# Kernel tuning notes

Measured on AMD Instinct MI355X. Metric: run time of the kernel, lower is better.

Reference implementation:

```python
import jax, jax.numpy as jnp
import numpy as np

B, C, N = 8, 512, 2048
C8 = C // 8


def setup_inputs() -> dict:
    key = jax.random.key(0)
    kx, kq, kk, kv, kg = jax.random.split(key, 5)
    return {
        "x": jax.random.normal(kx, (B, C, N), dtype=jnp.float32),
        "Wq": jax.random.normal(kq, (C8, C), dtype=jnp.float32) * (1.0 / np.sqrt(C)),
        "Wk": jax.random.normal(kk, (C8, C), dtype=jnp.float32) * (1.0 / np.sqrt(C)),
        "Wv": jax.random.normal(kv, (C, C), dtype=jnp.float32) * (1.0 / np.sqrt(C)),
        # torch init is gamma=0.0; use a small random value so the attention
        # branch contributes to the output.
        "gamma": jax.random.uniform(kg, (1,), dtype=jnp.float32),
    }


def reference(x, Wq, Wk, Wv, gamma):
    # 1x1 convs == per-position linear maps over channels
    f = jnp.einsum("oc,bcn->bon", Wq, x)   # [B, C/8, N]
    g = jnp.einsum("oc,bcn->bon", Wk, x)   # [B, C/8, N]
    h = jnp.einsum("oc,bcn->bon", Wv, x)   # [B, C,   N]
    # scores[b,n,m] = sum_c f[b,c,n] * g[b,c,m]  (unscaled, as in source)
    scores = jnp.einsum("bcn,bcm->bnm", f, g)  # [B, N, N]
    # softmax over dim=1 (the query-position axis) — atypical but faithful
    beta = jax.nn.softmax(scores, axis=1)
    # o = gamma * h @ beta + x
    o = gamma[0] * jnp.einsum("bcn,bnm->bcm", h, beta) + x
    return o
```

## Files before the change

### kernel.cpp

```cpp
#include <hip/hip_runtime.h>
#include <hip/hip_bf16.h>
#include <math.h>

#define NB 8
#define NC 512
#define NN 2048

typedef unsigned short u16;
typedef __attribute__((ext_vector_type(8))) short short8;
typedef __attribute__((ext_vector_type(4))) float f32x4;

__device__ __forceinline__ float bf16_to_f32(u16 v) {
  union { unsigned int u; float f; } c; c.u = ((unsigned int)v) << 16; return c.f;
}
__device__ __forceinline__ u16 f32_to_bf16(float f) {
  __hip_bfloat16 h = __float2bfloat16(f);
  union { __hip_bfloat16 h; u16 u; } c; c.h = h; return c.u;
}
__device__ __forceinline__ void split2(float v, unsigned short& hi, unsigned short& lo) {
  hi = f32_to_bf16(v);
  lo = f32_to_bf16(v - bf16_to_f32(hi));
}

__device__ __forceinline__ void gl_lds16(const void* g, void* l) {
  __builtin_amdgcn_global_load_lds(
      (const __attribute__((address_space(1))) unsigned int*)g,
      (__attribute__((address_space(3))) unsigned int*)l, 16, 0, 0);
}

__device__ __forceinline__ void stage128x32(const u16* __restrict__ src, size_t row_base,
                                            int selems, int k0, u16* lds, int tid) {
#pragma unroll
  for (int s = 0; s < 2; ++s) {
    int flat = s * 4096 + tid * 16;
    int row = flat >> 6;
    int kb  = flat & 63;
    const char* g = (const char*)(src + (row_base + row) * (size_t)selems + k0) + kb;
    u16* l = lds + s * 2048 + (tid & ~63) * 8;
    gl_lds16(g, l);
  }
}

__global__ __launch_bounds__(256)
void wsplit_kernel(const float* __restrict__ Wq, const float* __restrict__ Wk,
                   const float* __restrict__ Wv, u16* __restrict__ Whi,
                   u16* __restrict__ Wlo) {
  int idx = (blockIdx.x * 256 + threadIdx.x) * 4;
  int r = idx >> 9, c = idx & 511;
  const float* src;
  if (r < 64)       src = Wq + (size_t)r * NC + c;
  else if (r < 128) src = Wk + (size_t)(r - 64) * NC + c;
  else              src = Wv + (size_t)(r - 128) * NC + c;
  float4 v = *(const float4*)src;
  ushort4 hi, lo;
  split2(v.x, hi.x, lo.x); split2(v.y, hi.y, lo.y);
  split2(v.z, hi.z, lo.z); split2(v.w, hi.w, lo.w);
  *(ushort4*)&Whi[idx] = hi;
  *(ushort4*)&Wlo[idx] = lo;
}

__global__ __launch_bounds__(256)
void xsplit_kernel(const float* __restrict__ x, u16* __restrict__ xThi,
                   u16* __restrict__ xTlo) {
  const int b = blockIdx.z, c0 = blockIdx.y * 64, n0 = blockIdx.x * 64;
  __shared__ float t[64][65];
  const int tid = threadIdx.x, tx = tid & 15, ty = tid >> 4;
#pragma unroll
  for (int r = 0; r < 4; ++r) {
    int c = r * 16 + ty;
    float4 v = *(const float4*)&x[((size_t)b * NC + c0 + c) * NN + n0 + tx * 4];
    t[c][tx * 4 + 0] = v.x; t[c][tx * 4 + 1] = v.y;
    t[c][tx * 4 + 2] = v.z; t[c][tx * 4 + 3] = v.w;
  }
  __syncthreads();
#pragma unroll
  for (int r = 0; r < 4; ++r) {
    int n = r * 16 + ty;
    ushort4 hi, lo;
    split2(t[tx * 4 + 0][n], hi.x, lo.x);
    split2(t[tx * 4 + 1][n], hi.y, lo.y);
    split2(t[tx * 4 + 2][n], hi.z, lo.z);
    split2(t[tx * 4 + 3][n], hi.w, lo.w);
    size_t off = ((size_t)b * NN + n0 + n) * NC + c0 + tx * 4;
    *(ushort4*)&xThi[off] = hi;
    *(ushort4*)&xTlo[off] = lo;
  }
}

__global__ __launch_bounds__(256)
void proj_mfma_kernel(const u16* __restrict__ xThi, const u16* __restrict__ xTlo,
                      const u16* __restrict__ Whi, const u16* __restrict__ Wlo,
                      u16* __restrict__ fgThi, u16* __restrict__ fgTlo,
                      u16* __restrict__ hw) {
  const int b  = blockIdx.z;
  const int n0 = blockIdx.x * 128;
  const int r0 = blockIdx.y * 128;
  const bool fg = (r0 == 0);

  __shared__ u16 Wh[2][128 * 32], Wl[2][128 * 32], Xh[2][128 * 32], Xl[2][128 * 32];

  const int tid = threadIdx.x, wave = tid >> 6, lane = tid & 63;
  const int quad = lane >> 4, l16 = lane & 15;
  const int wa = (wave >> 1) * 64, wb = (wave & 1) * 64;
  const size_t xrow = (size_t)b * NN + n0;

  f32x4 acc[4][4];
#pragma unroll
  for (int i = 0; i < 4; ++i)
#pragma unroll
    for (int j = 0; j < 4; ++j) acc[i][j] = (f32x4){0.f, 0.f, 0.f, 0.f};

  stage128x32(Whi, r0, NC, 0, Wh[0], tid);
  stage128x32(xThi, xrow, NC, 0, Xh[0], tid);
  if (fg) {
    stage128x32(Wlo, r0, NC, 0, Wl[0], tid);
    stage128x32(xTlo, xrow, NC, 0, Xl[0], tid);
  }

  const int KIT = NC / 32;
  for (int ki = 0; ki < KIT; ++ki) {
    __syncthreads();
    if (ki + 1 < KIT) {
      const int nb = (ki + 1) & 1, k1 = (ki + 1) * 32;
      stage128x32(Whi, r0, NC, k1, Wh[nb], tid);
      stage128x32(xThi, xrow, NC, k1, Xh[nb], tid);
      if (fg) {
        stage128x32(Wlo, r0, NC, k1, Wl[nb], tid);
        stage128x32(xTlo, xrow, NC, k1, Xl[nb], tid);
      }
    }
    const int cur = ki & 1;

    if (fg) {
      short8 ah[4], al[4], bh[4], bl[4];
#pragma unroll
      for (int i = 0; i < 4; ++i) {
        ah[i] = *(short8*)&Wh[cur][(wa + i * 16 + l16) * 32 + quad * 8];
        al[i] = *(short8*)&Wl[cur][(wa + i * 16 + l16) * 32 + quad * 8];
      }
#pragma unroll
      for (int j = 0; j < 4; ++j) {
        bh[j] = *(short8*)&Xh[cur][(wb + j * 16 + l16) * 32 + quad * 8];
        bl[j] = *(short8*)&Xl[cur][(wb + j * 16 + l16) * 32 + quad * 8];
      }
#pragma unroll
      for (int i = 0; i < 4; ++i)
#pragma unroll
        for (int j = 0; j < 4; ++j) {
          acc[i][j] = __builtin_amdgcn_mfma_f32_16x16x32_bf16(ah[i], bh[j], acc[i][j], 0, 0, 0);
          acc[i][j] = __builtin_amdgcn_mfma_f32_16x16x32_bf16(ah[i], bl[j], acc[i][j], 0, 0, 0);
          acc[i][j] = __builtin_amdgcn_mfma_f32_16x16x32_bf16(al[i], bh[j], acc[i][j], 0, 0, 0);
        }
    } else {
      short8 ah[4], bh[4];
#pragma unroll
      for (int i = 0; i < 4; ++i)
        ah[i] = *(short8*)&Xh[cur][(wa + i * 16 + l16) * 32 + quad * 8];
#pragma unroll
      for (int j = 0; j < 4; ++j)
        bh[j] = *(short8*)&Wh[cur][(wb + j * 16 + l16) * 32 + quad * 8];
#pragma unroll
      for (int i = 0; i < 4; ++i)
#pragma unroll
        for (int j = 0; j < 4; ++j)
          acc[i][j] = __builtin_amdgcn_mfma_f32_16x16x32_bf16(ah[i], bh[j], acc[i][j], 0, 0, 0);
    }
  }

  if (fg) {
#pragma unroll
    for (int i = 0; i < 4; ++i)
#pragma unroll
      for (int j = 0; j < 4; ++j) {
        int rb = wa + i * 16 + quad * 4;
        int n  = n0 + wb + j * 16 + l16;
        ushort4 hi, lo;
        split2(acc[i][j][0], hi.x, lo.x); split2(acc[i][j][1], hi.y, lo.y);
        split2(acc[i][j][2], hi.z, lo.z); split2(acc[i][j][3], hi.w, lo.w);
        size_t off = ((size_t)b * NN + n) * 128 + rb;
        *(ushort4*)&fgThi[off] = hi;
        *(ushort4*)&fgTlo[off] = lo;
      }
  } else {
#pragma unroll
    for (int i = 0; i < 4; ++i)
#pragma unroll
      for (int j = 0; j < 4; ++j) {
        int nb = n0 + wa + i * 16 + quad * 4;
        int c  = r0 - 128 + wb + j * 16 + l16;
        ushort4 hi;
        hi.x = f32_to_bf16(acc[i][j][0]); hi.y = f32_to_bf16(acc[i][j][1]);
        hi.z = f32_to_bf16(acc[i][j][2]); hi.w = f32_to_bf16(acc[i][j][3]);
        *(ushort4*)&hw[((size_t)b * NC + c) * NN + nb] = hi;
      }
  }
}

__global__ __launch_bounds__(512, 4)
void attn_out_kernel(const u16* __restrict__ fgThi, const u16* __restrict__ fgTlo,
                     const u16* __restrict__ hw, const float* __restrict__ x,
                     const float* __restrict__ gamma, float* __restrict__ out) {
  const int s = blockIdx.x;
  const int xcd = s & 7;
  const int t = s >> 3;
  const int mt = t & 31;
  const int hi6 = t >> 5;
  const int combo = (hi6 << 3) | xcd;
  const int b = combo >> 1;
  const int ch = combo & 1;
  const int m0 = mt * 64;
  const int c0 = ch * 256;

  __shared__ u16 Fh[2][64 * 64], Fl[2][64 * 64];
  __shared__ u16 Hs[256 * 64];
  __shared__ u16 Ps[64 * 64];
  float* Dn = (float*)Ps;

  const int tid = threadIdx.x, wave = tid >> 6, lane = tid & 63;
  const int quad = lane >> 4, l16 = lane & 15;
  const int ws_n = (wave >> 2) * 32, ws_m = (wave & 3) * 16;
  const int wv_c = (wave >> 1) * 64, wv_m = (wave & 1) * 32;

  const size_t frow = (size_t)b * NN;
  const size_t hrow = (size_t)b * NC + c0;

  short8 gh[2], gl[2];
#pragma unroll
  for (int k = 0; k < 2; ++k) {
    size_t o = (frow + m0 + ws_m + l16) * 128 + 64 + k * 32 + quad * 8;
    gh[k] = *(const short8*)&fgThi[o];
    gl[k] = *(const short8*)&fgTlo[o];
  }

  {
    int flat = tid * 16;
    int row = flat >> 7, chunk = (flat >> 4) & 7;
    int kb = ((chunk ^ (row & 7)) << 4);
    gl_lds16((const char*)(fgThi + (frow + row) * 128) + kb, Fh[0] + (tid & ~63) * 8);
    gl_lds16((const char*)(fgTlo + (frow + row) * 128) + kb, Fl[0] + (tid & ~63) * 8);
#pragma unroll
    for (int s2 = 0; s2 < 4; ++s2) {
      int f2 = s2 * 8192 + tid * 16;
      int r2 = f2 >> 7, c2 = (f2 >> 4) & 7;
      gl_lds16((const char*)(hw + (hrow + r2) * NN) + ((c2 ^ (r2 & 7)) << 4),
               Hs + s2 * 4096 + (tid & ~63) * 8);
    }
  }
  __syncthreads();

  float dsum = 0.f;
  f32x4 ao[4][2];
#pragma unroll
  for (int i = 0; i < 4; ++i)
#pragma unroll
    for (int j = 0; j < 2; ++j) ao[i][j] = (f32x4){0.f, 0.f, 0.f, 0.f};

  const int NT = NN / 64;
  for (int it = 0; it < NT; ++it) {
    const int cur = it & 1;

    if (it > 0) {
      const int n1 = it * 64;
#pragma unroll
      for (int s2 = 0; s2 < 4; ++s2) {
        int f2 = s2 * 8192 + tid * 16;
        int r2 = f2 >> 7, c2 = (f2 >> 4) & 7;
        gl_lds16((const char*)(hw + (hrow + r2) * NN + n1) + ((c2 ^ (r2 & 7)) << 4),
                 Hs + s2 * 4096 + (tid & ~63) * 8);
      }
    }
    if (it + 1 < NT) {
      const int n1 = (it + 1) * 64;
      int flat = tid * 16;
      int row = flat >> 7, chunk = (flat >> 4) & 7;
      int kb = ((chunk ^ (row & 7)) << 4);
      gl_lds16((const char*)(fgThi + (frow + n1 + row) * 128) + kb,
               Fh[cur ^ 1] + (tid & ~63) * 8);
      gl_lds16((const char*)(fgTlo + (frow + n1 + row) * 128) + kb,
               Fl[cur ^ 1] + (tid & ~63) * 8);
    }

    f32x4 as[2];
#pragma unroll
    for (int i = 0; i < 2; ++i) as[i] = (f32x4){0.f, 0.f, 0.f, 0.f};
#pragma unroll
    for (int k = 0; k < 2; ++k) {
      short8 fh[2], fl[2];
#pragma unroll
      for (int i = 0; i < 2; ++i) {
        int rr = ws_n + i * 16 + l16;
        int ci = (((k * 4 + quad) ^ (rr & 7)) << 3);
        fh[i] = *(short8*)&Fh[cur][rr * 64 + ci];
        fl[i] = *(short8*)&Fl[cur][rr * 64 + ci];
      }
#pragma unroll
      for (int i = 0; i < 2; ++i) {
        as[i] = __builtin_amdgcn_mfma_f32_16x16x32_bf16(fh[i], gh[k], as[i], 0, 0, 0);
        as[i] = __builtin_amdgcn_mfma_f32_16x16x32_bf16(fh[i], gl[k], as[i], 0, 0, 0);
        as[i] = __builtin_amdgcn_mfma_f32_16x16x32_bf16(fl[i], gh[k], as[i], 0, 0, 0);
      }
    }

    {
      int m = ws_m + l16;
#pragma unroll
      for (int i = 0; i < 2; ++i) {
        float e0 = __expf(as[i][0]);
        float e1 = __expf(as[i][1]);
        float e2 = __expf(as[i][2]);
        float e3 = __expf(as[i][3]);
        dsum += (e0 + e1) + (e2 + e3);
        ushort4 pk;
        pk.x = f32_to_bf16(e0); pk.y = f32_to_bf16(e1);
        pk.z = f32_to_bf16(e2); pk.w = f32_to_bf16(e3);
        int nb = ws_n * 2 + i * 32 + quad * 8;
        int chunk = nb >> 4;
        int off = (nb & 15) >> 1;
        *(ushort4*)&Ps[m * 64 + ((chunk ^ (m & 7)) << 3) + off] = pk;
      }
    }

    if (it + 1 < NT) asm volatile("s_waitcnt vmcnt(2)" ::: "memory");
    else             asm volatile("s_waitcnt vmcnt(0)" ::: "memory");
    asm volatile("s_waitcnt lgkmcnt(0)" ::: "memory");
    __builtin_amdgcn_s_barrier();

#pragma unroll
    for (int k = 0; k < 2; ++k) {
      short8 hh[4], pb[2];
#pragma unroll
      for (int i = 0; i < 4; ++i) {
        int rr = wv_c + i * 16 + l16;
        hh[i] = *(short8*)&Hs[rr * 64 + ((((k * 4 + quad)) ^ (rr & 7)) << 3)];
      }
#pragma unroll
      for (int j = 0; j < 2; ++j) {
        int rm = wv_m + j * 16 + l16;
        pb[j] = *(short8*)&Ps[rm * 64 + ((((k * 4 + quad)) ^ (rm & 7)) << 3)];
      }
#pragma unroll
      for (int i = 0; i < 4; ++i)
#pragma unroll
        for (int j = 0; j < 2; ++j)
          ao[i][j] = __builtin_amdgcn_mfma_f32_16x16x32_bf16(hh[i], pb[j], ao[i][j], 0, 0, 0);
    }

    __syncthreads();
  }

  dsum += __shfl_xor(dsum, 16);
  dsum += __shfl_xor(dsum, 32);
  if (tid < 64) Dn[tid] = 0.f;
  __syncthreads();
  if (quad == 0) atomicAdd(&Dn[ws_m + l16], dsum);
  __syncthreads();

  const float g = gamma[0];
  float invd[2];
#pragma unroll
  for (int j = 0; j < 2; ++j)
    invd[j] = g / Dn[wv_m + j * 16 + l16];

#pragma unroll
  for (int i = 0; i < 4; ++i) {
#pragma unroll
    for (int j = 0; j < 2; ++j) {
      const int c = c0 + wv_c + i * 16 + quad * 4;
      const int m = m0 + wv_m + j * 16 + l16;
#pragma unroll
      for (int r = 0; r < 4; ++r) {
        size_t off = ((size_t)b * NC + c + r) * NN + m;
        out[off] = fmaf(invd[j], ao[i][j][r], x[off]);
      }
    }
  }
}

extern "C" void kernel_launch(void* const* d_in, const int* in_sizes, int n_in,
                              void* d_out, int out_size, void* d_ws, size_t ws_size,
                              hipStream_t stream) {
  const float* x     = (const float*)d_in[0];
  const float* Wq    = (const float*)d_in[1];
  const float* Wk    = (const float*)d_in[2];
  const float* Wv    = (const float*)d_in[3];
  const float* gamma = (const float*)d_in[4];
  float* out = (float*)d_out;

  char* ws = (char*)d_ws;
  u16*   xThi  = (u16*)ws;
  u16*   xTlo  = (u16*)(ws + 16777216);
  u16*   Whi   = (u16*)(ws + 33554432);
  u16*   Wlo   = (u16*)(ws + 34209792);
  u16*   fgThi = (u16*)(ws + 67108864);
  u16*   fgTlo = (u16*)(ws + 71303168);
  u16*   hw    = (u16*)(ws + 75497472);

  wsplit_kernel<<<dim3(320), 256, 0, stream>>>(Wq, Wk, Wv, Whi, Wlo);
  xsplit_kernel<<<dim3(NN / 64, NC / 64, NB), 256, 0, stream>>>(x, xThi, xTlo);
  proj_mfma_kernel<<<dim3(NN / 128, 5, NB), 256, 0, stream>>>(
      xThi, xTlo, Whi, Wlo, fgThi, fgTlo, hw);
  attn_out_kernel<<<dim3(512), 512, 0, stream>>>(fgThi, fgTlo, hw, x, gamma, out);
}
```

Measured before the change: 200.9 us.

## Cover all channels per attention block and load H directly into registers

Each attention block now handles all 512 channels for its 64 output positions instead of half, so the score/exp work per tile is no longer duplicated across two channel-halves. The grid is halved to 256 blocks. H tiles are read straight from global memory into registers rather than staged through LDS, which removes the H shared buffer and its async wait. The risks are higher register pressure from doubled accumulators (launch bounds lowered to 2 blocks), fewer blocks than CUs, and H global loads that are no longer prefetched ahead of use.

New measurement: 224.0 us. +11.5%, slower.

```diff
diff --git a/kernel.cpp b/kernel.cpp
--- a/kernel.cpp
+++ b/kernel.cpp
@@ -196,33 +196,26 @@
   }
 }
 
-__global__ __launch_bounds__(512, 4)
+__global__ __launch_bounds__(512, 2)
 void attn_out_kernel(const u16* __restrict__ fgThi, const u16* __restrict__ fgTlo,
                      const u16* __restrict__ hw, const float* __restrict__ x,
                      const float* __restrict__ gamma, float* __restrict__ out) {
   const int s = blockIdx.x;
-  const int xcd = s & 7;
-  const int t = s >> 3;
-  const int mt = t & 31;
-  const int hi6 = t >> 5;
-  const int combo = (hi6 << 3) | xcd;
-  const int b = combo >> 1;
-  const int ch = combo & 1;
+  const int b = s & 7;
+  const int mt = s >> 3;
   const int m0 = mt * 64;
-  const int c0 = ch * 256;
 
   __shared__ u16 Fh[2][64 * 64], Fl[2][64 * 64];
-  __shared__ u16 Hs[256 * 64];
   __shared__ u16 Ps[64 * 64];
   float* Dn = (float*)Ps;
 
   const int tid = threadIdx.x, wave = tid >> 6, lane = tid & 63;
   const int quad = lane >> 4, l16 = lane & 15;
   const int ws_n = (wave >> 2) * 32, ws_m = (wave & 3) * 16;
-  const int wv_c = (wave >> 1) * 64, wv_m = (wave & 1) * 32;
+  const int wv_c = wave * 64;
 
   const size_t frow = (size_t)b * NN;
-  const size_t hrow = (size_t)b * NC + c0;
+  const size_t hbase = (size_t)b * NC;
 
   short8 gh[2], gl[2];
 #pragma unroll
@@ -238,45 +231,37 @@
     int kb = ((chunk ^ (row & 7)) << 4);
     gl_lds16((const char*)(fgThi + (frow + row) * 128) + kb, Fh[0] + (tid & ~63) * 8);
     gl_lds16((const char*)(fgTlo + (frow + row) * 128) + kb, Fl[0] + (tid & ~63) * 8);
-#pragma unroll
-    for (int s2 = 0; s2 < 4; ++s2) {
-      int f2 = s2 * 8192 + tid * 16;
-      int r2 = f2 >> 7, c2 = (f2 >> 4) & 7;
-      gl_lds16((const char*)(hw + (hrow + r2) * NN) + ((c2 ^ (r2 & 7)) << 4),
-               Hs + s2 * 4096 + (tid & ~63) * 8);
-    }
   }
   __syncthreads();
 
   float dsum = 0.f;
-  f32x4 ao[4][2];
+  f32x4 ao[4][4];
 #pragma unroll
   for (int i = 0; i < 4; ++i)
 #pragma unroll
-    for (int j = 0; j < 2; ++j) ao[i][j] = (f32x4){0.f, 0.f, 0.f, 0.f};
+    for (int j = 0; j < 4; ++j) ao[i][j] = (f32x4){0.f, 0.f, 0.f, 0.f};
 
   const int NT = NN / 64;
   for (int it = 0; it < NT; ++it) {
     const int cur = it & 1;
-
-    if (it > 0) {
-      const int n1 = it * 64;
-#pragma unroll
-      for (int s2 = 0; s2 < 4; ++s2) {
-        int f2 = s2 * 8192 + tid * 16;
-        int r2 = f2 >> 7, c2 = (f2 >> 4) & 7;
-        gl_lds16((const char*)(hw + (hrow + r2) * NN + n1) + ((c2 ^ (r2 & 7)) << 4),
-                 Hs + s2 * 4096 + (tid & ~63) * 8);
-      }
-    }
+    const int n1 = it * 64;
+
+    short8 hreg[8];
+#pragma unroll
+    for (int i = 0; i < 4; ++i)
+#pragma unroll
+      for (int k = 0; k < 2; ++k)
+        hreg[i * 2 + k] = *(const short8*)&hw[
+            (hbase + wv_c + i * 16 + l16) * NN + n1 + (k * 4 + quad) * 8];
+
     if (it + 1 < NT) {
-      const int n1 = (it + 1) * 64;
+      const int nf = (it + 1) * 64;
       int flat = tid * 16;
       int row = flat >> 7, chunk = (flat >> 4) & 7;
       int kb = ((chunk ^ (row & 7)) << 4);
-      gl_lds16((const char*)(fgThi + (frow + n1 + row) * 128) + kb,
+      gl_lds16((const char*)(fgThi + (frow + nf + row) * 128) + kb,
                Fh[cur ^ 1] + (tid & ~63) * 8);
-      gl_lds16((const char*)(fgTlo + (frow + n1 + row) * 128) + kb,
+      gl_lds16((const char*)(fgTlo + (frow + nf + row) * 128) + kb,
                Fl[cur ^ 1] + (tid & ~63) * 8);
     }
 
@@ -320,29 +305,22 @@
       }
     }
 
-    if (it + 1 < NT) asm volatile("s_waitcnt vmcnt(2)" ::: "memory");
-    else             asm volatile("s_waitcnt vmcnt(0)" ::: "memory");
     asm volatile("s_waitcnt lgkmcnt(0)" ::: "memory");
     __builtin_amdgcn_s_barrier();
 
 #pragma unroll
     for (int k = 0; k < 2; ++k) {
-      short8 hh[4], pb[2];
-#pragma unroll
-      for (int i = 0; i < 4; ++i) {
-        int rr = wv_c + i * 16 + l16;
-        hh[i] = *(short8*)&Hs[rr * 64 + ((((k * 4 + quad)) ^ (rr & 7)) << 3)];
-      }
-#pragma unroll
-      for (int j = 0; j < 2; ++j) {
-        int rm = wv_m + j * 16 + l16;
+      short8 pb[4];
+#pragma unroll
+      for (int j = 0; j < 4; ++j) {
+        int rm = j * 16 + l16;
         pb[j] = *(short8*)&Ps[rm * 64 + ((((k * 4 + quad)) ^ (rm & 7)) << 3)];
       }
 #pragma unroll
       for (int i = 0; i < 4; ++i)
 #pragma unroll
-        for (int j = 0; j < 2; ++j)
-          ao[i][j] = __builtin_amdgcn_mfma_f32_16x16x32_bf16(hh[i], pb[j], ao[i][j], 0, 0, 0);
+        for (int j = 0; j < 4; ++j)
+          ao[i][j] = __builtin_amdgcn_mfma_f32_16x16x32_bf16(hreg[i * 2 + k], pb[j], ao[i][j], 0, 0, 0);
     }
 
     __syncthreads();
@@ -356,17 +334,17 @@
   __syncthreads();
 
   const float g = gamma[0];
-  float invd[2];
-#pragma unroll
-  for (int j = 0; j < 2; ++j)
-    invd[j] = g / Dn[wv_m + j * 16 + l16];
+  float invd[4];
+#pragma unroll
+  for (int j = 0; j < 4; ++j)
+    invd[j] = g / Dn[j * 16 + l16];
 
 #pragma unroll
   for (int i = 0; i < 4; ++i) {
 #pragma unroll
-    for (int j = 0; j < 2; ++j) {
-      const int c = c0 + wv_c + i * 16 + quad * 4;
-      const int m = m0 + wv_m + j * 16 + l16;
+    for (int j = 0; j < 4; ++j) {
+      const int c = wv_c + i * 16 + quad * 4;
+      const int m = m0 + j * 16 + l16;
 #pragma unroll
       for (int r = 0; r < 4; ++r) {
         size_t off = ((size_t)b * NC + c + r) * NN + m;
@@ -399,5 +377,5 @@
   xsplit_kernel<<<dim3(NN / 64, NC / 64, NB), 256, 0, stream>>>(x, xThi, xTlo);
   proj_mfma_kernel<<<dim3(NN / 128, 5, NB), 256, 0, stream>>>(
       xThi, xTlo, Whi, Wlo, fgThi, fgTlo, hw);
-  attn_out_kernel<<<dim3(512), 512, 0, stream>>>(fgThi, fgTlo, hw, x, gamma, out);
-}
+  attn_out_kernel<<<dim3(256), 512, 0, stream>>>(fgThi, fgTlo, hw, x, gamma, out);
+}
```

## Fuse x transpose/bf16 split into projection kernel staging

Applied to the files above, without the earlier changes.

Removes the separate xsplit kernel that wrote transposed hi/lo bf16 copies of x to global memory. The projection kernel now loads fp32 x directly, converts and transposes it in registers, and writes it to a swizzled LDS layout. The next tile's loads are issued before the MFMA work and written to LDS afterward to overlap. This saves a kernel launch and about 32MB of global write+read traffic, at the cost of scalar 2-byte LDS stores and redundant conversion across the 5 row-blocks that share the same x tile.

Measured after the change: 214.0 us. +6.6%, slower.

```diff
diff --git a/kernel.cpp b/kernel.cpp
--- a/kernel.cpp
+++ b/kernel.cpp
@@ -60,35 +60,7 @@
 }
 
 __global__ __launch_bounds__(256)
-void xsplit_kernel(const float* __restrict__ x, u16* __restrict__ xThi,
-                   u16* __restrict__ xTlo) {
-  const int b = blockIdx.z, c0 = blockIdx.y * 64, n0 = blockIdx.x * 64;
-  __shared__ float t[64][65];
-  const int tid = threadIdx.x, tx = tid & 15, ty = tid >> 4;
-#pragma unroll
-  for (int r = 0; r < 4; ++r) {
-    int c = r * 16 + ty;
-    float4 v = *(const float4*)&x[((size_t)b * NC + c0 + c) * NN + n0 + tx * 4];
-    t[c][tx * 4 + 0] = v.x; t[c][tx * 4 + 1] = v.y;
-    t[c][tx * 4 + 2] = v.z; t[c][tx * 4 + 3] = v.w;
-  }
-  __syncthreads();
-#pragma unroll
-  for (int r = 0; r < 4; ++r) {
-    int n = r * 16 + ty;
-    ushort4 hi, lo;
-    split2(t[tx * 4 + 0][n], hi.x, lo.x);
-    split2(t[tx * 4 + 1][n], hi.y, lo.y);
-    split2(t[tx * 4 + 2][n], hi.z, lo.z);
-    split2(t[tx * 4 + 3][n], hi.w, lo.w);
-    size_t off = ((size_t)b * NN + n0 + n) * NC + c0 + tx * 4;
-    *(ushort4*)&xThi[off] = hi;
-    *(ushort4*)&xTlo[off] = lo;
-  }
-}
-
-__global__ __launch_bounds__(256)
-void proj_mfma_kernel(const u16* __restrict__ xThi, const u16* __restrict__ xTlo,
+void proj_mfma_kernel(const float* __restrict__ x,
                       const u16* __restrict__ Whi, const u16* __restrict__ Wlo,
                       u16* __restrict__ fgThi, u16* __restrict__ fgTlo,
                       u16* __restrict__ hw) {
@@ -102,7 +74,38 @@
   const int tid = threadIdx.x, wave = tid >> 6, lane = tid & 63;
   const int quad = lane >> 4, l16 = lane & 15;
   const int wa = (wave >> 1) * 64, wb = (wave & 1) * 64;
-  const size_t xrow = (size_t)b * NN + n0;
+
+  const int cN = tid & 31;
+  const int cC = tid >> 5;
+
+  f32x4 xr[4];
+  auto loadX = [&](int k0) {
+#pragma unroll
+    for (int p = 0; p < 4; ++p) {
+      int c = p * 8 + cC;
+      xr[p] = *(const f32x4*)&x[((size_t)b * NC + k0 + c) * NN + n0 + cN * 4];
+    }
+  };
+  auto writeX = [&](u16* XhD, u16* XlD, bool dolo) {
+#pragma unroll
+    for (int p = 0; p < 4; ++p) {
+      int c = p * 8 + cC;
+      int cc = c >> 3, ce = c & 7;
+#pragma unroll
+      for (int i = 0; i < 4; ++i) {
+        int n = cN * 4 + i;
+        int addr = n * 32 + ((cc ^ ((n >> 2) & 3)) << 3) + ce;
+        if (dolo) {
+          unsigned short hi, lo;
+          split2(xr[p][i], hi, lo);
+          XhD[addr] = hi;
+          XlD[addr] = lo;
+        } else {
+          XhD[addr] = f32_to_bf16(xr[p][i]);
+        }
+      }
+    }
+  };
 
   f32x4 acc[4][4];
 #pragma unroll
@@ -111,25 +114,21 @@
     for (int j = 0; j < 4; ++j) acc[i][j] = (f32x4){0.f, 0.f, 0.f, 0.f};
 
   stage128x32(Whi, r0, NC, 0, Wh[0], tid);
-  stage128x32(xThi, xrow, NC, 0, Xh[0], tid);
-  if (fg) {
-    stage128x32(Wlo, r0, NC, 0, Wl[0], tid);
-    stage128x32(xTlo, xrow, NC, 0, Xl[0], tid);
-  }
+  if (fg) stage128x32(Wlo, r0, NC, 0, Wl[0], tid);
+  loadX(0);
+  writeX(Xh[0], Xl[0], fg);
 
   const int KIT = NC / 32;
   for (int ki = 0; ki < KIT; ++ki) {
     __syncthreads();
+    const int cur = ki & 1;
+    const int nb  = cur ^ 1;
     if (ki + 1 < KIT) {
-      const int nb = (ki + 1) & 1, k1 = (ki + 1) * 32;
+      const int k1 = (ki + 1) * 32;
       stage128x32(Whi, r0, NC, k1, Wh[nb], tid);
-      stage128x32(xThi, xrow, NC, k1, Xh[nb], tid);
-      if (fg) {
-        stage128x32(Wlo, r0, NC, k1, Wl[nb], tid);
-        stage128x32(xTlo, xrow, NC, k1, Xl[nb], tid);
-      }
-    }
-    const int cur = ki & 1;
+      if (fg) stage128x32(Wlo, r0, NC, k1, Wl[nb], tid);
+      loadX(k1);
+    }
 
     if (fg) {
       short8 ah[4], al[4], bh[4], bl[4];
@@ -140,8 +139,10 @@
       }
 #pragma unroll
       for (int j = 0; j < 4; ++j) {
-        bh[j] = *(short8*)&Xh[cur][(wb + j * 16 + l16) * 32 + quad * 8];
-        bl[j] = *(short8*)&Xl[cur][(wb + j * 16 + l16) * 32 + quad * 8];
+        int rr = wb + j * 16 + l16;
+        int ci = ((quad ^ ((rr >> 2) & 3)) << 3);
+        bh[j] = *(short8*)&Xh[cur][rr * 32 + ci];
+        bl[j] = *(short8*)&Xl[cur][rr * 32 + ci];
       }
 #pragma unroll
       for (int i = 0; i < 4; ++i)
@@ -154,8 +155,11 @@
     } else {
       short8 ah[4], bh[4];
 #pragma unroll
-      for (int i = 0; i < 4; ++i)
-        ah[i] = *(short8*)&Xh[cur][(wa + i * 16 + l16) * 32 + quad * 8];
+      for (int i = 0; i < 4; ++i) {
+        int rr = wa + i * 16 + l16;
+        int ci = ((quad ^ ((rr >> 2) & 3)) << 3);
+        ah[i] = *(short8*)&Xh[cur][rr * 32 + ci];
+      }
 #pragma unroll
       for (int j = 0; j < 4; ++j)
         bh[j] = *(short8*)&Wh[cur][(wb + j * 16 + l16) * 32 + quad * 8];
@@ -165,6 +169,8 @@
         for (int j = 0; j < 4; ++j)
           acc[i][j] = __builtin_amdgcn_mfma_f32_16x16x32_bf16(ah[i], bh[j], acc[i][j], 0, 0, 0);
     }
+
+    if (ki + 1 < KIT) writeX(Xh[nb], Xl[nb], fg);
   }
 
   if (fg) {
@@ -186,12 +192,12 @@
     for (int i = 0; i < 4; ++i)
 #pragma unroll
       for (int j = 0; j < 4; ++j) {
-        int nb = n0 + wa + i * 16 + quad * 4;
+        int nb2 = n0 + wa + i * 16 + quad * 4;
         int c  = r0 - 128 + wb + j * 16 + l16;
         ushort4 hi;
         hi.x = f32_to_bf16(acc[i][j][0]); hi.y = f32_to_bf16(acc[i][j][1]);
         hi.z = f32_to_bf16(acc[i][j][2]); hi.w = f32_to_bf16(acc[i][j][3]);
-        *(ushort4*)&hw[((size_t)b * NC + c) * NN + nb] = hi;
+        *(ushort4*)&hw[((size_t)b * NC + c) * NN + nb2] = hi;
       }
   }
 }
@@ -387,8 +393,6 @@
   float* out = (float*)d_out;
 
   char* ws = (char*)d_ws;
-  u16*   xThi  = (u16*)ws;
-  u16*   xTlo  = (u16*)(ws + 16777216);
   u16*   Whi   = (u16*)(ws + 33554432);
   u16*   Wlo   = (u16*)(ws + 34209792);
   u16*   fgThi = (u16*)(ws + 67108864);
@@ -396,8 +400,7 @@
   u16*   hw    = (u16*)(ws + 75497472);
 
   wsplit_kernel<<<dim3(320), 256, 0, stream>>>(Wq, Wk, Wv, Whi, Wlo);
-  xsplit_kernel<<<dim3(NN / 64, NC / 64, NB), 256, 0, stream>>>(x, xThi, xTlo);
   proj_mfma_kernel<<<dim3(NN / 128, 5, NB), 256, 0, stream>>>(
-      xThi, xTlo, Whi, Wlo, fgThi, fgTlo, hw);
+      x, Whi, Wlo, fgThi, fgTlo, hw);
   attn_out_kernel<<<dim3(512), 512, 0, stream>>>(fgThi, fgTlo, hw, x, gamma, out);
 }
```
